# Kernel tuning notes

Measured on AMD Instinct MI355X. Metric: run time of the kernel, lower is better.

Reference implementation:

```python
import jax, jax.numpy as jnp
import numpy as np

B, L, V, E = 4096, 200, 100000, 50  # users, max ratings per user, movie vocab, embedding size


def setup_inputs() -> dict:
    key = jax.random.key(0)
    ks = jax.random.split(key, 10)
    emb = jax.random.normal(ks[0], (V, E), jnp.float32) * 0.1
    user_movie_idx = jax.random.randint(ks[1], (B, L), 0, V)
    lengths = jax.random.randint(ks[2], (B,), 1, L + 1)  # at least 1 rating per user
    ratings = jax.random.uniform(ks[3], (B, L), jnp.float32, 0.5, 5.0)
    movie_idx = jax.random.randint(ks[4], (B,), 0, V)

    def lin(k, fan_in, fan_out):
        bound = 1.0 / np.sqrt(fan_in)
        return jax.random.uniform(k, (fan_in, fan_out), jnp.float32, -bound, bound)

    W1 = lin(ks[5], 5 * E, 2 * E)
    b1 = jnp.zeros((2 * E,), jnp.float32)
    W2 = lin(ks[6], 2 * E, E)
    b2 = jnp.zeros((E,), jnp.float32)
    W3 = lin(ks[7], E, 1)
    b3 = jnp.zeros((1,), jnp.float32)
    return dict(emb=emb, ratings=ratings, W1=W1, b1=b1, W2=W2, b2=b2, W3=W3, b3=b3,
                user_movie_idx=user_movie_idx, lengths=lengths, movie_idx=movie_idx)


def reference(emb, ratings, W1, b1, W2, b2, W3, b3, user_movie_idx, lengths, movie_idx):
    # ragged per-user weighted gather: [B, L, E]
    mask = (jnp.arange(L)[None, :] < lengths[:, None])  # [B, L] valid positions
    w = emb[user_movie_idx] * ratings[:, :, None]
    m = mask[:, :, None]
    inf = jnp.float32(jnp.inf)

    wmin = jnp.min(jnp.where(m, w, inf), axis=1)          # [B, E]
    wmax = jnp.max(jnp.where(m, w, -inf), axis=1)         # [B, E]
    n = lengths[:, None].astype(w.dtype)
    wmean = jnp.sum(jnp.where(m, w, 0.0), axis=1) / n     # [B, E]
    # torch median = lower median: sorted index (n-1)//2; pad with +inf so it sorts last
    ws = jnp.sort(jnp.where(m, w, inf), axis=1)
    med_idx = jnp.broadcast_to(((lengths - 1) // 2)[:, None, None], (B, 1, E))
    wmed = jnp.take_along_axis(ws, med_idx, axis=1)[:, 0, :]  # [B, E]

    u = jnp.concatenate([wmin, wmax, wmean, wmed], axis=1)  # [B, 4E]
    u = u / jnp.linalg.norm(u, axis=1, keepdims=True)

    x = jnp.concatenate([u, emb[movie_idx]], axis=1)        # [B, 5E]
    h = jax.nn.relu(x @ W1 + b1)   # dropout is identity in eval
    h = jax.nn.relu(h @ W2 + b2)
    return jax.nn.sigmoid(h @ W3 + b3)  # [B, 1]
```

## Files before the change

kernel.cpp:

```cpp
#include <hip/hip_runtime.h>
#include <math.h>

#define NB 4096
#define LL 200
#define EE 50
#define LP 201
#define NT 512
#define GG 8
#define IT 25
#define SW 8

#define K2B 256
#define K2T 512
#define BPB 16

__device__ __forceinline__ unsigned f2key(float f) {
    unsigned b = __float_as_uint(f);
    unsigned mask = (b & 0x80000000u) ? 0xFFFFFFFFu : 0x80000000u;
    return b ^ mask;
}
__device__ __forceinline__ float key2f(unsigned kk) {
    unsigned mask = (kk & 0x80000000u) ? 0x80000000u : 0xFFFFFFFFu;
    return __uint_as_float(kk ^ mask);
}

__device__ __forceinline__ unsigned select_median(
    int n, int k, int g, int grp, const unsigned it[IT],
    unsigned kmin, unsigned kmax, unsigned (*sbuf)[SW], int *scnt)
{
    unsigned LO = kmin, HI = kmax + 1u;
    int cLO = 0, cHI = n;
    unsigned med = 0u;
    bool small = false;
    int pass = 0;
    for (;;) {
        if (HI - LO == 1u) { med = LO; break; }
        const int w = cHI - cLO;
        if (w <= SW) { small = true; break; }
        unsigned P;
        if (pass < 8) {
            const float vlo = key2f(LO);
            const float vhi = key2f(HI - 1u);
            const float frac = (float)(k - cLO + 1) / (float)(w + 1);
            P = f2key(vlo + (vhi - vlo) * frac);
        } else {
            P = LO + ((HI - LO) >> 1);
        }
        if (P <= LO) P = LO + 1u;
        if (P >= HI) P = HI - 1u;
        int c = 0;
        #pragma unroll
        for (int t = 0; t < IT; t++) c += (it[t] < P) ? 1 : 0;
        c += __shfl_xor(c, 1);
        c += __shfl_xor(c, 2);
        c += __shfl_xor(c, 4);
        if (c > k) { HI = P; cHI = c; }
        else       { LO = P; cLO = c; }
        pass++;
    }
    if (small) {
        const int w = cHI - cLO;
        const int r = k - cLO;
        #pragma unroll
        for (int t = 0; t < IT; t++) {
            const unsigned kk = it[t];
            if (kk >= LO && kk < HI) {
                const int pos = atomicAdd(&scnt[grp], 1);
                if (pos < SW) sbuf[grp][pos] = kk;
            }
        }
        const unsigned sv = (g < w) ? sbuf[grp][g] : 0xFFFFFFFFu;
        int cLess = 0, cLeq = 0;
        for (int j = 0; j < w; j++) {
            const unsigned o = sbuf[grp][j];
            cLess += (o <  sv) ? 1 : 0;
            cLeq  += (o <= sv) ? 1 : 0;
        }
        unsigned cand = (g < w && cLess <= r && r < cLeq) ? sv : 0xFFFFFFFFu;
        #pragma unroll
        for (int m2 = 1; m2 < GG; m2 <<= 1)
            cand = min(cand, (unsigned)__shfl_xor((int)cand, m2));
        med = cand;
    }
    return med;
}

extern "C" __global__ void __launch_bounds__(NT, 6)
rec_stats(const float* __restrict__ emb, const float* __restrict__ ratings,
          const int* __restrict__ uidx, const int* __restrict__ lens,
          float* __restrict__ uo)
{
    __shared__ unsigned wK[EE][LP];
    __shared__ int      idxL[LL];
    __shared__ float    ratL[LL];
    __shared__ unsigned sbuf[NT/GG][SW];
    __shared__ int      scnt[NT/GG];

    const int b   = blockIdx.x;
    const int tid = threadIdx.x;
    const int n   = lens[b];
    const int k   = (n - 1) >> 1;

    if (tid < NT/GG) scnt[tid] = 0;
    if (tid < n) {
        idxL[tid] = uidx[b*LL + tid];
        ratL[tid] = ratings[b*LL + tid];
    }
    __syncthreads();

    if (tid < 20 * (EE/2)) {
        const int e2 = tid % (EE/2);
        int l        = tid / (EE/2);
        for (; l < n; l += 20) {
            const float2 ev = ((const float2*)emb)[(size_t)idxL[l]*(EE/2) + e2];
            const float  r  = ratL[l];
            wK[2*e2    ][l] = f2key(ev.x * r);
            wK[2*e2 + 1][l] = f2key(ev.y * r);
        }
    }
    __syncthreads();

    const int f = tid >> 3;
    const int g = tid & 7;

    if (f < EE) {
        unsigned raw[IT];
        #pragma unroll
        for (int t = 0; t < IT; t++) raw[t] = wK[f][g + (t << 3)];

        unsigned it[IT];
        unsigned kmin = 0xFFFFFFFFu, kmax = 0u;
        float sm = 0.f;
        #pragma unroll
        for (int t = 0; t < IT; t++) {
            const int l = g + (t << 3);
            unsigned kk = 0xFFFFFFFFu;
            if (l < n) {
                kk = raw[t];
                kmin = min(kmin, kk);
                kmax = max(kmax, kk);
                sm += key2f(kk);
            }
            it[t] = kk;
        }
        #pragma unroll
        for (int m2 = 1; m2 < GG; m2 <<= 1) {
            kmin = min(kmin, (unsigned)__shfl_xor((int)kmin, m2));
            kmax = max(kmax, (unsigned)__shfl_xor((int)kmax, m2));
            sm  += __shfl_xor(sm, m2);
        }

        const unsigned med = select_median(n, k, g, f, it, kmin, kmax,
                                           sbuf, scnt);
        if (g == 0) {
            float* ub = uo + (size_t)b * (4*EE);
            ub[f]        = key2f(kmin);
            ub[EE + f]   = key2f(kmax);
            ub[2*EE + f] = sm / (float)n;
            ub[3*EE + f] = key2f(med);
        }
    }
}

extern "C" __global__ void __launch_bounds__(K2T, 2)
rec_mlp(const float* __restrict__ emb,
        const float* __restrict__ W1, const float* __restrict__ b1,
        const float* __restrict__ W2, const float* __restrict__ b2,
        const float* __restrict__ W3, const float* __restrict__ b3,
        const int* __restrict__ midx, const float* __restrict__ uo,
        float* __restrict__ out)
{
    __shared__ float W1s[5*EE * 2*EE];
    __shared__ float W2s[2*EE * EE];
    __shared__ float b1s[2*EE];
    __shared__ float b2s[EE];
    __shared__ float W3s[EE];
    __shared__ float xs[8][252];

    const int tid = threadIdx.x;

    for (int p = tid; p < (5*EE*2*EE)/2; p += K2T)
        ((float2*)W1s)[p] = ((const float2*)W1)[p];
    for (int p = tid; p < (2*EE*EE)/2; p += K2T)
        ((float2*)W2s)[p] = ((const float2*)W2)[p];
    if (tid < 2*EE) b1s[tid] = b1[tid];
    if (tid < EE)   { b2s[tid] = b2[tid]; W3s[tid] = W3[tid]; }
    __syncthreads();
    const float bias3 = b3[0];

    const int w    = tid >> 6;
    const int lane = tid & 63;

    #pragma unroll
    for (int rep = 0; rep < 2; rep++) {
        const int b = blockIdx.x * BPB + rep * 8 + w;

        float uv0 = 0.f, uv1 = 0.f, uv2 = 0.f, uv3 = 0.f;
        const float* ub = uo + (size_t)b * (4*EE);
        uv0 = ub[lane];
        uv1 = ub[lane + 64];
        uv2 = ub[lane + 128];
        if (lane < 4*EE - 192) uv3 = ub[lane + 192];
        float v2 = uv0*uv0 + uv1*uv1 + uv2*uv2 + uv3*uv3;
        #pragma unroll
        for (int m2 = 1; m2 < 64; m2 <<= 1) v2 += __shfl_xor(v2, m2);
        const float inv = 1.0f / sqrtf(v2);

        xs[w][lane]       = uv0 * inv;
        xs[w][lane + 64]  = uv1 * inv;
        xs[w][lane + 128] = uv2 * inv;
        if (lane < 4*EE - 192) xs[w][lane + 192] = uv3 * inv;
        if (lane < EE) xs[w][4*EE + lane] = emb[(size_t)midx[b]*EE + lane];
        asm volatile("s_waitcnt lgkmcnt(0)" ::: "memory");

        const int o2 = (lane + 64 < 2*EE) ? lane + 64 : 2*EE - 1;
        float a0 = 0.f, a1 = 0.f;
        #pragma unroll 5
        for (int i = 0; i < 5*EE; i++) {
            const float xv = xs[w][i];
            a0 += xv * W1s[i*(2*EE) + lane];
            a1 += xv * W1s[i*(2*EE) + o2];
        }
        const float h0  = fmaxf(a0 + b1s[lane], 0.f);
        const float h64 = fmaxf(a1 + b1s[o2],   0.f);
        xs[w][lane] = h0;
        if (lane < 2*EE - 64) xs[w][lane + 64] = h64;
        asm volatile("s_waitcnt lgkmcnt(0)" ::: "memory");

        const int oc = (lane < EE) ? lane : EE - 1;
        float a2 = 0.f;
        #pragma unroll 5
        for (int i = 0; i < 2*EE; i++)
            a2 += xs[w][i] * W2s[i*EE + oc];
        const float h2v = fmaxf(a2 + b2s[oc], 0.f);
        float v = (lane < EE) ? h2v * W3s[lane] : 0.f;
        #pragma unroll
        for (int m2 = 1; m2 < 64; m2 <<= 1) v += __shfl_xor(v, m2);
        if (lane == 0) out[b] = 1.0f / (1.0f + expf(-(v + bias3)));
    }
}

extern "C" void kernel_launch(void* const* d_in, const int* in_sizes, int n_in,
                              void* d_out, int out_size, void* d_ws, size_t ws_size,
                              hipStream_t stream) {
    const float* emb     = (const float*)d_in[0];
    const float* ratings = (const float*)d_in[1];
    const float* W1      = (const float*)d_in[2];
    const float* b1      = (const float*)d_in[3];
    const float* W2      = (const float*)d_in[4];
    const float* b2      = (const float*)d_in[5];
    const float* W3      = (const float*)d_in[6];
    const float* b3      = (const float*)d_in[7];
    const int*   uidx    = (const int*)d_in[8];
    const int*   lens    = (const int*)d_in[9];
    const int*   midx    = (const int*)d_in[10];
    float* out = (float*)d_out;
    float* uo  = (float*)d_ws;

    hipLaunchKernelGGL(rec_stats, dim3(NB), dim3(NT), 0, stream,
                       emb, ratings, uidx, lens, uo);
    hipLaunchKernelGGL(rec_mlp, dim3(K2B), dim3(K2T), 0, stream,
                       emb, W1, b1, W2, b2, W3, b3, midx, uo, out);
}
```

Baseline: 101.5 us.

## Halve stats LDS buffer via two-phase chunked gather and fold min/max/sum into gather

The per-user key buffer is cut to about half the columns and filled in two chunks, with each thread pulling its register slice between chunks. The smaller LDS footprint allows a higher launch-bounds occupancy target (8 instead of 6). Sum, min and max are now accumulated during the gather and reduced from per-thread partials, so that pass is removed from the median phase. It adds an extra block barrier and a second gather pass, and uses a hardware reciprocal when picking the median pivot.

```diff
diff --git a/kernel.cpp b/kernel.cpp
--- a/kernel.cpp
+++ b/kernel.cpp
@@ -4,10 +4,12 @@
 #define NB 4096
 #define LL 200
 #define EE 50
-#define LP 201
+#define CH 104
+#define CP 105
 #define NT 512
 #define GG 8
 #define IT 25
+#define IT1 13
 #define SW 8
 
 #define K2B 256
@@ -22,6 +24,13 @@
 __device__ __forceinline__ float key2f(unsigned kk) {
     unsigned mask = (kk & 0x80000000u) ? 0x80000000u : 0xFFFFFFFFu;
     return __uint_as_float(kk ^ mask);
+}
+__device__ __forceinline__ float fastrcp(float x) {
+#if __has_builtin(__builtin_amdgcn_rcpf)
+    return __builtin_amdgcn_rcpf(x);
+#else
+    return 1.0f / x;
+#endif
 }
 
 __device__ __forceinline__ unsigned select_median(
@@ -41,7 +50,7 @@
         if (pass < 8) {
             const float vlo = key2f(LO);
             const float vhi = key2f(HI - 1u);
-            const float frac = (float)(k - cLO + 1) / (float)(w + 1);
+            const float frac = (float)(k - cLO + 1) * fastrcp((float)(w + 1));
             P = f2key(vlo + (vhi - vlo) * frac);
         } else {
             P = LO + ((HI - LO) >> 1);
@@ -85,12 +94,15 @@
     return med;
 }
 
-extern "C" __global__ void __launch_bounds__(NT, 6)
+extern "C" __global__ void __launch_bounds__(NT, 8)
 rec_stats(const float* __restrict__ emb, const float* __restrict__ ratings,
           const int* __restrict__ uidx, const int* __restrict__ lens,
           float* __restrict__ uo)
 {
-    __shared__ unsigned wK[EE][LP];
+    __shared__ unsigned wK[EE][CP];
+    __shared__ float    ps [EE][20];
+    __shared__ float    pmn[EE][20];
+    __shared__ float    pmx[EE][20];
     __shared__ int      idxL[LL];
     __shared__ float    ratL[LL];
     __shared__ unsigned sbuf[NT/GG][SW];
@@ -108,14 +120,27 @@
     }
     __syncthreads();
 
-    if (tid < 20 * (EE/2)) {
-        const int e2 = tid % (EE/2);
-        int l        = tid / (EE/2);
-        for (; l < n; l += 20) {
-            const float2 ev = ((const float2*)emb)[(size_t)idxL[l]*(EE/2) + e2];
-            const float  r  = ratL[l];
-            wK[2*e2    ][l] = f2key(ev.x * r);
-            wK[2*e2 + 1][l] = f2key(ev.y * r);
+    const int  e2 = tid % (EE/2);
+    const int  l0 = tid / (EE/2);
+    const bool gv = tid < 20 * (EE/2);
+
+    float sA = 0.f, sB = 0.f;
+    float mnA = INFINITY, mxA = -INFINITY, mnB = INFINITY, mxB = -INFINITY;
+
+    if (gv) {
+        for (int col = l0; col < CH; col += 20) {
+            if (col < n) {
+                const float2 ev = ((const float2*)emb)[(size_t)idxL[col]*(EE/2) + e2];
+                const float  r  = ratL[col];
+                const float  a  = ev.x * r, c = ev.y * r;
+                wK[2*e2    ][col] = f2key(a);
+                wK[2*e2 + 1][col] = f2key(c);
+                sA += a; mnA = fminf(mnA, a); mxA = fmaxf(mxA, a);
+                sB += c; mnB = fminf(mnB, c); mxB = fmaxf(mxB, c);
+            } else {
+                wK[2*e2    ][col] = 0xFFFFFFFFu;
+                wK[2*e2 + 1][col] = 0xFFFFFFFFu;
+            }
         }
     }
     __syncthreads();
@@ -123,40 +148,63 @@
     const int f = tid >> 3;
     const int g = tid & 7;
 
+    unsigned it[IT];
     if (f < EE) {
-        unsigned raw[IT];
-        #pragma unroll
-        for (int t = 0; t < IT; t++) raw[t] = wK[f][g + (t << 3)];
-
-        unsigned it[IT];
-        unsigned kmin = 0xFFFFFFFFu, kmax = 0u;
-        float sm = 0.f;
-        #pragma unroll
-        for (int t = 0; t < IT; t++) {
-            const int l = g + (t << 3);
-            unsigned kk = 0xFFFFFFFFu;
+        #pragma unroll
+        for (int t = 0; t < IT1; t++) it[t] = wK[f][g + (t << 3)];
+    }
+    __syncthreads();
+
+    if (gv) {
+        for (int col = l0; col < LL - CH; col += 20) {
+            const int l = CH + col;
             if (l < n) {
-                kk = raw[t];
-                kmin = min(kmin, kk);
-                kmax = max(kmax, kk);
-                sm += key2f(kk);
+                const float2 ev = ((const float2*)emb)[(size_t)idxL[l]*(EE/2) + e2];
+                const float  r  = ratL[l];
+                const float  a  = ev.x * r, c = ev.y * r;
+                wK[2*e2    ][col] = f2key(a);
+                wK[2*e2 + 1][col] = f2key(c);
+                sA += a; mnA = fminf(mnA, a); mxA = fmaxf(mxA, a);
+                sB += c; mnB = fminf(mnB, c); mxB = fmaxf(mxB, c);
+            } else {
+                wK[2*e2    ][col] = 0xFFFFFFFFu;
+                wK[2*e2 + 1][col] = 0xFFFFFFFFu;
             }
-            it[t] = kk;
+        }
+        ps [2*e2][l0] = sA;  ps [2*e2+1][l0] = sB;
+        pmn[2*e2][l0] = mnA; pmn[2*e2+1][l0] = mnB;
+        pmx[2*e2][l0] = mxA; pmx[2*e2+1][l0] = mxB;
+    }
+    __syncthreads();
+
+    if (f < EE) {
+        #pragma unroll
+        for (int t = IT1; t < IT; t++) it[t] = wK[f][(g + (t << 3)) - CH];
+
+        float s  = ps [f][g] + ps [f][g+8];
+        float mn = fminf(pmn[f][g], pmn[f][g+8]);
+        float mx = fmaxf(pmx[f][g], pmx[f][g+8]);
+        if (g < 4) {
+            s += ps[f][g+16];
+            mn = fminf(mn, pmn[f][g+16]);
+            mx = fmaxf(mx, pmx[f][g+16]);
         }
         #pragma unroll
         for (int m2 = 1; m2 < GG; m2 <<= 1) {
-            kmin = min(kmin, (unsigned)__shfl_xor((int)kmin, m2));
-            kmax = max(kmax, (unsigned)__shfl_xor((int)kmax, m2));
-            sm  += __shfl_xor(sm, m2);
-        }
+            s  += __shfl_xor(s, m2);
+            mn  = fminf(mn, __shfl_xor(mn, m2));
+            mx  = fmaxf(mx, __shfl_xor(mx, m2));
+        }
+        const unsigned kmin = f2key(mn);
+        const unsigned kmax = f2key(mx);
 
         const unsigned med = select_median(n, k, g, f, it, kmin, kmax,
                                            sbuf, scnt);
         if (g == 0) {
             float* ub = uo + (size_t)b * (4*EE);
-            ub[f]        = key2f(kmin);
-            ub[EE + f]   = key2f(kmax);
-            ub[2*EE + f] = sm / (float)n;
+            ub[f]        = mn;
+            ub[EE + f]   = mx;
+            ub[2*EE + f] = s / (float)n;
             ub[3*EE + f] = key2f(med);
         }
     }
```

New measurement: 93.70 us. -7.7%, faster.
